# Performance work log

Measured on AMD Instinct MI355X. Metric: run time of the kernel, lower is better.

Reference implementation:

```python
import jax, jax.numpy as jnp
import numpy as np

B, T, D = 16, 2048, 1024


def setup_inputs() -> dict:
    key = jax.random.key(0)
    k1, k2, k3 = jax.random.split(key, 3)
    # scale k and w so the cumulative exp-decay state stays finite in fp32
    k = jax.random.normal(k1, (B, T, D), dtype=jnp.float32) * 0.5
    v = jax.random.normal(k2, (B, T, D), dtype=jnp.float32)
    w = jax.random.normal(k3, (B, T, D), dtype=jnp.float32) * 0.05 - 0.1
    return {"k": k, "v": v, "w": w}


def reference(k, v, w):
    # RWKV-style WKV recurrence, unrolled over the time axis with lax.scan.
    #   a_t = exp(w_t) * a_{t-1} + exp(k_t)
    #   b_t = exp(w_t) * b_{t-1} + exp(k_t) * v_t
    #   out_t = b_t / a_t
    # k, v, w: [B, T, D]; state a, b: [B, D]; initial state zeros (torch buffers).
    ek = jnp.exp(k)
    ew = jnp.exp(w)

    def step(carry, xs):
        a, b = carry
        ew_t, ek_t, v_t = xs  # each [B, D]
        a = ew_t * a + ek_t
        b = ew_t * b + ek_t * v_t
        return (a, b), b / a

    xs = (ew.transpose(1, 0, 2), ek.transpose(1, 0, 2), v.transpose(1, 0, 2))  # [T, B, D]
    bsz, _, dim = k.shape
    init = (jnp.zeros((bsz, dim), dtype=k.dtype), jnp.zeros((bsz, dim), dtype=k.dtype))
    _, out = jax.lax.scan(step, init, xs)  # out: [T, B, D]
    return out.transpose(1, 0, 2)  # [B, T, D]
```

## Files before the change

kernel.cpp:

```cpp
#include <hip/hip_runtime.h>


#define TT 2048
#define DD 1024
#define UU 16

__global__ __launch_bounds__(64) void wkv_fwd(const float* __restrict__ kg,
                                              const float* __restrict__ vg,
                                              const float* __restrict__ wg,
                                              float* __restrict__ og) {
    const int c = blockIdx.x * 64 + threadIdx.x;
    const size_t base = (size_t)(c >> 10) * (size_t)TT * DD
                      + (size_t)(c & (DD - 1));
    const float* kp = kg + base;
    const float* vp = vg + base;
    const float* wp = wg + base;
    float*       op = og + base;

    float kA[UU], vA[UU], wA[UU];
    float kB[UU], vB[UU], wB[UU];

#pragma unroll
    for (int j = 0; j < UU; ++j) {
        const size_t off = (size_t)j * DD;
        kA[j] = kp[off];
        vA[j] = vp[off];
        wA[j] = wp[off];
    }

    float a = 0.0f, b = 0.0f;

    for (int t0 = 0; t0 < TT; t0 += 2 * UU) {
#pragma unroll
        for (int j = 0; j < UU; ++j) {
            const size_t off = (size_t)(t0 + UU + j) * DD;
            kB[j] = kp[off];
            vB[j] = vp[off];
            wB[j] = wp[off];
        }
#pragma unroll
        for (int j = 0; j < UU; ++j) {
            const float ew = __expf(wA[j]);
            const float ek = __expf(kA[j]);
            a = ew * a + ek;
            b = ew * b + ek * vA[j];
            op[(size_t)(t0 + j) * DD] = __fdividef(b, a);
        }
        if (t0 + 2 * UU < TT) {
#pragma unroll
            for (int j = 0; j < UU; ++j) {
                const size_t off = (size_t)(t0 + 2 * UU + j) * DD;
                kA[j] = kp[off];
                vA[j] = vp[off];
                wA[j] = wp[off];
            }
        }
#pragma unroll
        for (int j = 0; j < UU; ++j) {
            const float ew = __expf(wB[j]);
            const float ek = __expf(kB[j]);
            a = ew * a + ek;
            b = ew * b + ek * vB[j];
            op[(size_t)(t0 + UU + j) * DD] = __fdividef(b, a);
        }
    }
}

extern "C" void kernel_launch(void* const* d_in, const int* in_sizes, int n_in,
                              void* d_out, int out_size, void* d_ws, size_t ws_size,
                              hipStream_t stream) {
    const float* k = (const float*)d_in[0];
    const float* v = (const float*)d_in[1];
    const float* w = (const float*)d_in[2];
    float* out = (float*)d_out;

    const int channels = 16 * DD;
    wkv_fwd<<<dim3(channels / 64), dim3(64), 0, stream>>>(k, v, w, out);
}
```

Measured before the change: 485.2 us.

## Parallelize WKV recurrence over time with chunked scan and decoupled lookback

Replaces the one-thread-per-channel sequential scan with a chunked parallel scan. Each block takes a dynamic ticket for a (channel tile, time super-chunk) pair. Four warps each reduce a 32-step segment into an affine (P, A, B) summary, and the block combines these in shared memory. The incoming state is obtained from the previous super-chunk through flag-based serial lookback in global workspace, and each warp then replays its segment to write outputs. This exposes far more parallelism than the original 256 wavefronts, which underfill the GPU. In exchange it adds a memset, atomics, spin-waiting on global flags, and an inter-chunk dependency chain. Output precision shifts slightly because state is recombined via the products P.

Result: slower. 644.8 us (+32.9%).

```diff
diff --git a/kernel.cpp b/kernel.cpp
--- a/kernel.cpp
+++ b/kernel.cpp
@@ -1,68 +1,123 @@
 #include <hip/hip_runtime.h>
 
 
-#define TT 2048
-#define DD 1024
-#define UU 16
+#define T_LEN 2048
+#define D_LEN 1024
+#define B_SZ  16
+#define LSTEP 32
+#define UCH   4
+#define SUPER (T_LEN / (LSTEP * UCH))
+#define NTILE (B_SZ * D_LEN / 64)
+#define NBLK  (NTILE * SUPER)
 
-__global__ __launch_bounds__(64) void wkv_fwd(const float* __restrict__ kg,
-                                              const float* __restrict__ vg,
-                                              const float* __restrict__ wg,
-                                              float* __restrict__ og) {
-    const int c = blockIdx.x * 64 + threadIdx.x;
-    const size_t base = (size_t)(c >> 10) * (size_t)TT * DD
-                      + (size_t)(c & (DD - 1));
-    const float* kp = kg + base;
-    const float* vp = vg + base;
-    const float* wp = wg + base;
-    float*       op = og + base;
+static_assert(NTILE == 256, "ticket decode assumes NTILE=256");
 
-    float kA[UU], vA[UU], wA[UU];
-    float kB[UU], vB[UU], wB[UU];
+__global__ __launch_bounds__(256, 4) void wkv_scan(const float* __restrict__ kg,
+                                                   const float* __restrict__ vg,
+                                                   const float* __restrict__ wg,
+                                                   float* __restrict__ og,
+                                                   unsigned* __restrict__ counter,
+                                                   unsigned* __restrict__ flags,
+                                                   float* __restrict__ inc) {
+    __shared__ unsigned s_ticket;
+    __shared__ float s_part[UCH][3][64];
+    __shared__ float s_in[3][64];
 
+    const int ch = threadIdx.x;
+    const int u  = threadIdx.y;
+
+    if (ch == 0 && u == 0) s_ticket = atomicAdd(counter, 1u);
+    __syncthreads();
+    const unsigned ticket = s_ticket;
+    const int tile = (int)(ticket & (NTILE - 1));
+    const int s    = (int)(ticket >> 8);
+
+    const int chain = tile * 64 + ch;
+    const int bidx  = chain >> 10;
+    const int d     = chain & (D_LEN - 1);
+    const int t0    = s * (LSTEP * UCH) + u * LSTEP;
+    const size_t base = (size_t)bidx * T_LEN * D_LEN + (size_t)t0 * D_LEN + d;
+
+    float ew[LSTEP], ek[LSTEP], ekv[LSTEP];
+    float P = 1.0f, A = 0.0f, Bb = 0.0f;
 #pragma unroll
-    for (int j = 0; j < UU; ++j) {
-        const size_t off = (size_t)j * DD;
-        kA[j] = kp[off];
-        vA[j] = vp[off];
-        wA[j] = wp[off];
+    for (int j = 0; j < LSTEP; ++j) {
+        const size_t off = base + (size_t)j * D_LEN;
+        const float kj = kg[off];
+        const float vj = vg[off];
+        const float wj = wg[off];
+        const float e1 = __expf(wj);
+        const float e2 = __expf(kj);
+        ew[j]  = e1;
+        ek[j]  = e2;
+        ekv[j] = e2 * vj;
+        P *= e1;
+        A  = e1 * A  + e2;
+        Bb = e1 * Bb + ekv[j];
     }
 
-    float a = 0.0f, b = 0.0f;
+    s_part[u][0][ch] = P;
+    s_part[u][1][ch] = A;
+    s_part[u][2][ch] = Bb;
+    __syncthreads();
 
-    for (int t0 = 0; t0 < TT; t0 += 2 * UU) {
+    if (u == 0) {
+        float Pf = s_part[0][0][ch], Af = s_part[0][1][ch], Bf = s_part[0][2][ch];
 #pragma unroll
-        for (int j = 0; j < UU; ++j) {
-            const size_t off = (size_t)(t0 + UU + j) * DD;
-            kB[j] = kp[off];
-            vB[j] = vp[off];
-            wB[j] = wp[off];
+        for (int q = 1; q < UCH; ++q) {
+            const float Pq = s_part[q][0][ch];
+            const float Aq = s_part[q][1][ch];
+            const float Bq = s_part[q][2][ch];
+            Af = Pq * Af + Aq;
+            Bf = Pq * Bf + Bq;
+            Pf = Pf * Pq;
         }
+
+        float Pin = 1.0f, Ain = 0.0f, Bin = 0.0f;
+        if (s > 0) {
+            const int fidx = tile * SUPER + (s - 1);
+            while (__hip_atomic_load(&flags[fidx], __ATOMIC_ACQUIRE,
+                                     __HIP_MEMORY_SCOPE_AGENT) == 0u) {
+                __builtin_amdgcn_s_sleep(2);
+            }
+            const size_t ib = (size_t)fidx * 192;
+            Pin = inc[ib + 0 * 64 + ch];
+            Ain = inc[ib + 1 * 64 + ch];
+            Bin = inc[ib + 2 * 64 + ch];
+        }
+
+        if (s < SUPER - 1) {
+            const int   oidx = tile * SUPER + s;
+            const size_t ob  = (size_t)oidx * 192;
+            inc[ob + 0 * 64 + ch] = Pin * Pf;
+            inc[ob + 1 * 64 + ch] = Pf * Ain + Af;
+            inc[ob + 2 * 64 + ch] = Pf * Bin + Bf;
+            __hip_atomic_store(&flags[oidx], 1u, __ATOMIC_RELEASE,
+                               __HIP_MEMORY_SCOPE_AGENT);
+        }
+
+        s_in[0][ch] = Pin;
+        s_in[1][ch] = Ain;
+        s_in[2][ch] = Bin;
+    }
+    __syncthreads();
+
+    float Ai = s_in[1][ch], Bi = s_in[2][ch];
 #pragma unroll
-        for (int j = 0; j < UU; ++j) {
-            const float ew = __expf(wA[j]);
-            const float ek = __expf(kA[j]);
-            a = ew * a + ek;
-            b = ew * b + ek * vA[j];
-            op[(size_t)(t0 + j) * DD] = __fdividef(b, a);
+    for (int q = 0; q < UCH - 1; ++q) {
+        if (q < u) {
+            const float Pq = s_part[q][0][ch];
+            Ai = Pq * Ai + s_part[q][1][ch];
+            Bi = Pq * Bi + s_part[q][2][ch];
         }
-        if (t0 + 2 * UU < TT) {
+    }
+
+    float a = Ai, b = Bi;
 #pragma unroll
-            for (int j = 0; j < UU; ++j) {
-                const size_t off = (size_t)(t0 + 2 * UU + j) * DD;
-                kA[j] = kp[off];
-                vA[j] = vp[off];
-                wA[j] = wp[off];
-            }
-        }
-#pragma unroll
-        for (int j = 0; j < UU; ++j) {
-            const float ew = __expf(wB[j]);
-            const float ek = __expf(kB[j]);
-            a = ew * a + ek;
-            b = ew * b + ek * vB[j];
-            op[(size_t)(t0 + UU + j) * DD] = __fdividef(b, a);
-        }
+    for (int j = 0; j < LSTEP; ++j) {
+        a = ew[j] * a + ek[j];
+        b = ew[j] * b + ekv[j];
+        og[base + (size_t)j * D_LEN] = __fdividef(b, a);
     }
 }
 
@@ -74,6 +129,12 @@
     const float* w = (const float*)d_in[2];
     float* out = (float*)d_out;
 
-    const int channels = 16 * DD;
-    wkv_fwd<<<dim3(channels / 64), dim3(64), 0, stream>>>(k, v, w, out);
+    unsigned* counter = (unsigned*)d_ws;
+    unsigned* flags   = (unsigned*)((char*)d_ws + 256);
+    float*    inc     = (float*)((char*)d_ws + 256 + NBLK * sizeof(unsigned));
+
+    hipMemsetAsync(d_ws, 0, 256 + NBLK * sizeof(unsigned), stream);
+
+    wkv_scan<<<dim3(NBLK), dim3(64, UCH), 0, stream>>>(k, v, w, out,
+                                                       counter, flags, inc);
 }
```
